# Kernel optimization log

Hardware: AMD Instinct MI355X
Metric: run time of the kernel (lower is better)

Reference implementation:

```python
import jax, jax.numpy as jnp
import numpy as np

RADIUS = 0.8
NSAMPLE = 32
EPS = 1e-5  # BatchNorm eps


def _bn(x, gamma, beta, axes):
    # BatchNorm (training-mode batch statistics), channel dim kept via broadcasting
    m = jnp.mean(x, axis=axes, keepdims=True)
    v = jnp.var(x, axis=axes, keepdims=True)
    return (x - m) * jax.lax.rsqrt(v + EPS) * gamma + beta


def setup_inputs() -> dict:
    key = jax.random.key(0)
    ks = jax.random.split(key, 6)
    B, N, P, C, COUT = 4, 8192, 2048, 128, 256
    ffps_xyz = jax.random.uniform(ks[0], (B, P, 3), dtype=jnp.float32) * 2.0 - 1.0
    backbone_xyz = jax.random.uniform(ks[1], (B, N, 3), dtype=jnp.float32) * 2.0 - 1.0
    backbone_features = jax.random.normal(ks[2], (B, C, N), dtype=jnp.float32)
    w_shift = jax.random.normal(ks[3], (3, 3), dtype=jnp.float32) * 0.1
    gamma_shift = jnp.ones((3,), jnp.float32)
    beta_shift = jnp.zeros((3,), jnp.float32)
    w_mlp = jax.random.normal(ks[4], (COUT, 3 + C), dtype=jnp.float32) * 0.05
    gamma_mlp = jnp.ones((COUT,), jnp.float32)
    beta_mlp = jnp.zeros((COUT,), jnp.float32)
    return {
        "ffps_xyz": ffps_xyz,
        "backbone_xyz": backbone_xyz,
        "backbone_features": backbone_features,
        "w_shift": w_shift,
        "gamma_shift": gamma_shift,
        "beta_shift": beta_shift,
        "w_mlp": w_mlp,
        "gamma_mlp": gamma_mlp,
        "beta_mlp": beta_mlp,
    }


def reference(ffps_xyz, backbone_xyz, backbone_features,
              w_shift, gamma_shift, beta_shift,
              w_mlp, gamma_mlp, beta_mlp):
    B, P, _ = ffps_xyz.shape
    N = backbone_xyz.shape[1]

    # ---- shift_layer: Conv1d(3->3, k=1, no bias) + BN1d + ReLU on (B,3,P) ----
    x = jnp.einsum('oc,bpc->bop', w_shift, ffps_xyz)                  # (B,3,P)
    x = _bn(x, gamma_shift[None, :, None], beta_shift[None, :, None], (0, 2))
    new_xyz = jax.nn.relu(x).transpose(0, 2, 1)                       # (B,P,3) query centers

    # ---- QueryAndGroup: ball query (radius, nsample), use_xyz=True ----
    d2 = jnp.sum((new_xyz[:, :, None, :] - backbone_xyz[:, None, :, :]) ** 2, -1)  # (B,P,N)
    within = d2 < (RADIUS * RADIUS)
    # pick the first NSAMPLE in-radius indices (CUDA ball_query semantics)
    keyv = jnp.where(within, jnp.arange(N, dtype=jnp.int32), jnp.int32(N))
    negk, idx = jax.lax.top_k(-keyv, NSAMPLE)                          # smallest keys first
    valid = (-negk) < N
    idx = jnp.where(valid, idx, idx[..., :1])                          # pad with first found idx

    g_xyz = jnp.take_along_axis(backbone_xyz[:, None, :, :], idx[..., None], axis=2)
    g_xyz = g_xyz - new_xyz[:, :, None, :]                             # (B,P,S,3) recentered
    feats = backbone_features.transpose(0, 2, 1)                       # (B,N,C)
    g_f = jnp.take_along_axis(feats[:, None, :, :], idx[..., None], axis=2)  # (B,P,S,C)
    g = jnp.concatenate([g_xyz, g_f], axis=-1)                         # (B,P,S,3+C)

    # ---- mlp: 1x1 conv (3+C -> COUT, no bias) + BN + ReLU ----
    y = jnp.einsum('oc,bpsc->bops', w_mlp, g)                          # (B,COUT,P,S)
    y = _bn(y, gamma_mlp[None, :, None, None], beta_mlp[None, :, None, None], (0, 2, 3))
    y = jax.nn.relu(y)

    # ---- max-pool over neighbor axis, squeeze, transpose ----
    y = jnp.max(y, axis=3)                                             # (B,COUT,P)
    return y.transpose(0, 2, 1)                                        # (B,P,COUT)
```

## Files before the change

kernel.cpp:

```cpp
#include <hip/hip_runtime.h>
#include <math.h>

namespace {
constexpr int B    = 4;
constexpr int N    = 8192;
constexpr int P    = 2048;
constexpr int C    = 128;
constexpr int COUT = 256;
constexpr int NS   = 32;
constexpr int BP   = B * P;
constexpr int BPB  = 2;
constexpr int GRP  = 8;
constexpr int NBLK = (BP / (BPB * GRP)) * 2;

constexpr size_t OFF_FEATT = 0;
constexpr size_t OFF_WSWZ  = 8388608;
constexpr size_t OFF_SSLOT = 8470528;
constexpr size_t OFF_SUMS  = 8471040;
constexpr size_t OFF_IDX   = 8475136;
constexpr size_t OFF_GX    = 9523712;
constexpr size_t OFF_YMAX  = 11620864;
constexpr size_t WS_NEED   = 20009472;
}

typedef short bf16x8 __attribute__((ext_vector_type(8)));
typedef float f32x4  __attribute__((ext_vector_type(4)));

typedef const __attribute__((address_space(1))) void gas_void;
typedef __attribute__((address_space(3))) void las_void;
#define GLOBAL_LOAD_LDS16(gp, lp) \
    __builtin_amdgcn_global_load_lds((gas_void*)(gp), (las_void*)(lp), 16, 0, 0)

__device__ inline unsigned short f2bf(float f) {
    unsigned u = __float_as_uint(f);
    unsigned r = u + 0x7fffu + ((u >> 16) & 1u);
    return (unsigned short)(r >> 16);
}

__global__ __launch_bounds__(256) void k_prep(const float* __restrict__ ffps,
                                              const float* __restrict__ wsh,
                                              double* __restrict__ sslot,
                                              float* __restrict__ sums) {
#pragma clang fp contract(off)
    int blk = blockIdx.x, t = threadIdx.x;
    if (blk == 8) {
        ((f32x4*)sums)[t & 127] = (f32x4){0.f, 0.f, 0.f, 0.f};
        return;
    }
    __shared__ double red[6][256];
    double w[9];
#pragma unroll
    for (int i = 0; i < 9; i++) w[i] = (double)wsh[i];
    double s[3] = {0, 0, 0}, sq[3] = {0, 0, 0};
#pragma unroll
    for (int i = 0; i < 4; i++) {
        int p = blk * 1024 + t + 256 * i;
        double f0 = (double)ffps[p * 3 + 0];
        double f1 = (double)ffps[p * 3 + 1];
        double f2 = (double)ffps[p * 3 + 2];
#pragma unroll
        for (int o = 0; o < 3; o++) {
            double xo = (w[o * 3 + 0] * f0 + w[o * 3 + 1] * f1) + w[o * 3 + 2] * f2;
            s[o] += xo;
            sq[o] += xo * xo;
        }
    }
#pragma unroll
    for (int o = 0; o < 3; o++) { red[o][t] = s[o]; red[3 + o][t] = sq[o]; }
    for (int off = 128; off > 0; off >>= 1) {
        __syncthreads();
        if (t < off) {
#pragma unroll
            for (int j = 0; j < 6; j++) red[j][t] += red[j][t + off];
        }
    }
    __syncthreads();
    if (t < 6) sslot[blk * 6 + t] = red[t][0];
}

__global__ __launch_bounds__(256) void k_front(const float* __restrict__ ffps,
                                               const float* __restrict__ bbxyz,
                                               const float* __restrict__ feat,
                                               const float* __restrict__ wsh,
                                               const float* __restrict__ gsh,
                                               const float* __restrict__ bsh,
                                               const float* __restrict__ wml,
                                               const double* __restrict__ sslot,
                                               unsigned short* __restrict__ featT,
                                               unsigned short* __restrict__ wswz,
                                               int* __restrict__ idxo,
                                               uint2* __restrict__ gxo) {
#pragma clang fp contract(off)
    int blk = blockIdx.x, t = threadIdx.x;
    if (blk >= 2048) {
        int rb = blk - 2048;
        if (rb < 2048) {
            __shared__ float tile[64][33];
            int tx = t & 31, ty = t >> 5;
            int n0 = (rb & 255) * 32, c0 = ((rb >> 8) & 1) * 64, b = rb >> 9;
            const float* src = feat + ((size_t)b * C + c0) * N + n0;
#pragma unroll
            for (int j = 0; j < 8; j++) tile[ty + 8 * j][tx] = src[(size_t)(ty + 8 * j) * N + tx];
            __syncthreads();
            int n = t >> 3;
            int k8 = (t & 7) * 8;
            unsigned vv[4];
#pragma unroll
            for (int i = 0; i < 4; i++) {
                unsigned lo = f2bf(tile[k8 + 2 * i][n]);
                unsigned hi = f2bf(tile[k8 + 2 * i + 1][n]);
                vv[i] = lo | (hi << 16);
            }
            *(int4*)&featT[((size_t)b * N + n0 + n) * C + c0 + k8] =
                make_int4((int)vv[0], (int)vv[1], (int)vv[2], (int)vv[3]);
        } else {
            int i = (rb - 2048) * 256 + t;
            int j = i & 7;
            int lane = (i >> 3) & 63;
            int rest = i >> 9;
            int ks = rest % 5, rt = rest / 5;
            int cout = rt * 16 + (lane & 15);
            int k = ks * 32 + (lane >> 4) * 8 + j;
            float v = 0.f;
            if (k < 128) v = wml[cout * 131 + 3 + k];
            else if (k < 131) v = wml[cout * 131 + (k - 128)];
            wswz[i] = f2bf(v);
        }
        return;
    }

    __shared__ double spar[6];
    if (t < 6) {
        double a = 0.0;
        for (int r = 0; r < 8; r++) a += sslot[r * 6 + t];
        spar[t] = a;
    }
    __syncthreads();
    int wv = t >> 6, lane = t & 63;
    int q = blk * 4 + wv;
    int b = q >> 11;
    double f0 = (double)ffps[q * 3 + 0];
    double f1 = (double)ffps[q * 3 + 1];
    double f2 = (double)ffps[q * 3 + 2];
    double qd[3];
#pragma unroll
    for (int o = 0; o < 3; o++) {
        double m  = spar[o] * (1.0 / 8192.0);
        double v  = spar[3 + o] * (1.0 / 8192.0) - m * m;
        double is = 1.0 / sqrt(v + 1e-5);
        double x  = ((double)wsh[o * 3 + 0] * f0 + (double)wsh[o * 3 + 1] * f1) +
                    (double)wsh[o * 3 + 2] * f2;
        double y  = ((x - m) * is) * (double)gsh[o] + (double)bsh[o];
        qd[o] = (y > 0.0) ? y : 0.0;
    }
    double qx = qd[0], qy = qd[1], qz = qd[2];
    float cfx = (float)qx, cfy = (float)qy, cfz = (float)qz;
    const float* base = bbxyz + (size_t)b * N * 3;
    const double R2 = 0.8 * 0.8;
    const float R2F = 0.64f;
    {
        double ex = fmax(fmax(qx - 1.0, -1.0 - qx), 0.0);
        double ey = fmax(fmax(qy - 1.0, -1.0 - qy), 0.0);
        double ez = fmax(fmax(qz - 1.0, -1.0 - qz), 0.0);
        if (ex * ex + ey * ey + ez * ez >= R2) {
            if (lane < NS) {
                idxo[q * NS + lane] = 0;
                float rx = base[0] - cfx, ry = base[1] - cfy, rz = base[2] - cfz;
                unsigned u01 = (unsigned)f2bf(rx) | ((unsigned)f2bf(ry) << 16);
                gxo[q * NS + lane] = make_uint2(u01, (unsigned)f2bf(rz));
            }
            return;
        }
    }
    int found = 0, firstn = -1;

    float X0[8], Y0[8], Z0[8], X1[8], Y1[8], Z1[8], X2[8], Y2[8], Z2[8];

    auto loadb = [&](float (&XX)[8], float (&YY)[8], float (&ZZ)[8], int it) {
#pragma unroll
        for (int j = 0; j < 8; j++) {
            int n = it * 512 + j * 64 + lane;
            XX[j] = base[n * 3 + 0];
            YY[j] = base[n * 3 + 1];
            ZZ[j] = base[n * 3 + 2];
        }
    };
    auto proc = [&](float (&XX)[8], float (&YY)[8], float (&ZZ)[8], int it) {
#pragma clang fp contract(off)
#pragma unroll
        for (int j = 0; j < 8; j++) {
            int n = it * 512 + j * 64 + lane;
            float dxf = cfx - XX[j];
            float dyf = cfy - YY[j];
            float dzf = cfz - ZZ[j];
            float d2f = (dxf * dxf + dyf * dyf) + dzf * dzf;
            bool within;
            if (__builtin_expect(fabsf(d2f - R2F) < 1e-4f, 0)) {
                double dx = qx - (double)XX[j];
                double dy = qy - (double)YY[j];
                double dz = qz - (double)ZZ[j];
                within = ((dx * dx + dy * dy) + dz * dz) < R2;
            } else {
                within = d2f < R2F;
            }
            unsigned long long mask = __ballot(within);
            if (firstn < 0 && mask != 0ull) firstn = (n - lane) + (__ffsll(mask) - 1);
            if (within) {
                int rank = found + __popcll(mask & ((1ull << lane) - 1ull));
                if (rank < NS) {
                    idxo[q * NS + rank] = n;
                    float rx = XX[j] - cfx, ry = YY[j] - cfy, rz = ZZ[j] - cfz;
                    unsigned u01 = (unsigned)f2bf(rx) | ((unsigned)f2bf(ry) << 16);
                    gxo[q * NS + rank] = make_uint2(u01, (unsigned)f2bf(rz));
                }
            }
            found += __popcll(mask);
        }
    };

    loadb(X0, Y0, Z0, 0);
    loadb(X1, Y1, Z1, 1);
    loadb(X2, Y2, Z2, 2);

    for (int itb = 0; itb < 16; itb += 3) {
        proc(X0, Y0, Z0, itb);
        if (found >= NS) break;
        loadb(X0, Y0, Z0, (itb + 3 < 16) ? itb + 3 : 0);
        if (itb + 1 >= 16) break;
        proc(X1, Y1, Z1, itb + 1);
        if (found >= NS) break;
        loadb(X1, Y1, Z1, (itb + 4 < 16) ? itb + 4 : 0);
        if (itb + 2 >= 16) break;
        proc(X2, Y2, Z2, itb + 2);
        if (found >= NS) break;
        loadb(X2, Y2, Z2, (itb + 5 < 16) ? itb + 5 : 0);
    }
    if (found < NS) {
        int padv = (found == 0) ? 0 : firstn;
        if (lane >= found && lane < NS) {
            idxo[q * NS + lane] = padv;
            float rx = base[padv * 3 + 0] - cfx;
            float ry = base[padv * 3 + 1] - cfy;
            float rz = base[padv * 3 + 2] - cfz;
            unsigned u01 = (unsigned)f2bf(rx) | ((unsigned)f2bf(ry) << 16);
            gxo[q * NS + lane] = make_uint2(u01, (unsigned)f2bf(rz));
        }
    }
}

__global__ __launch_bounds__(256, 4) void k_mlp_mfma(
        const unsigned short* __restrict__ featT,
        const unsigned short* __restrict__ wswz,
        const int* __restrict__ idx,
        const uint2* __restrict__ gxyz,
        float* __restrict__ ymax,
        float* __restrict__ sums) {
    __shared__ alignas(16) unsigned short G[2][4 * 4 * 64 * 8];
    int t = threadIdx.x, lane = t & 63, w = t >> 6;
    int q = lane >> 4, c16 = lane & 15;
    int blk = blockIdx.x;
    int nh = blk & 1;
    int bpbase = (blk >> 1) * (BPB * GRP);
    const bf16x8* wp = (const bf16x8*)wswz;

    bf16x8 wreg[5][2];
#pragma unroll
    for (int ks = 0; ks < 5; ks++)
#pragma unroll
        for (int nt = 0; nt < 2; nt++)
            wreg[ks][nt] = wp[((nh * 8 + w * 2 + nt) * 5 + ks) * 64 + lane];

    int sOff = (w >> 1) * NS + (w & 1) * 16 + c16;
    size_t fb = (size_t)(bpbase >> 11) * N * C;

    int nS0 = idx[bpbase * NS + sOff] & (N - 1);
    int nS1 = idx[(bpbase + BPB) * NS + sOff] & (N - 1);
    uint2 gx_c[4] = {}, gx_n[4] = {};
    if (q == 0)
#pragma unroll
        for (int mt = 0; mt < 4; mt++)
            gx_c[mt] = gxyz[(bpbase + (mt >> 1)) * NS + (mt & 1) * 16 + c16];
    {
        const unsigned short* row = featT + fb + (size_t)nS0 * C + q * 8;
#pragma unroll
        for (int ks = 0; ks < 4; ks++)
            GLOBAL_LOAD_LDS16(row + ks * 32, &G[0][(w * 4 + ks) * 512]);
    }

    float smA[2] = {0.f, 0.f}, sqA[2] = {0.f, 0.f};

    for (int g = 0; g < GRP; g++) {
        int buf = g & 1;
        int bp0 = bpbase + g * BPB;
        __syncthreads();
        if (g + 1 < GRP) {
            const unsigned short* row = featT + fb + (size_t)nS1 * C + q * 8;
#pragma unroll
            for (int ks = 0; ks < 4; ks++)
                GLOBAL_LOAD_LDS16(row + ks * 32, &G[buf ^ 1][(w * 4 + ks) * 512]);
            if (q == 0)
#pragma unroll
                for (int mt = 0; mt < 4; mt++)
                    gx_n[mt] = gxyz[(bp0 + BPB + (mt >> 1)) * NS + (mt & 1) * 16 + c16];
        }
        if (g + 2 < GRP) nS0 = idx[(bp0 + 2 * BPB) * NS + sOff] & (N - 1);

        f32x4 acc[4][2];
#pragma unroll
        for (int mt = 0; mt < 4; mt++)
#pragma unroll
            for (int nt = 0; nt < 2; nt++) acc[mt][nt] = (f32x4){0.f, 0.f, 0.f, 0.f};

#pragma unroll
        for (int ks = 0; ks < 4; ks++) {
            bf16x8 ag[4];
#pragma unroll
            for (int mt = 0; mt < 4; mt++)
                ag[mt] = *(const bf16x8*)&G[buf][((mt * 4 + ks) * 64 + lane) * 8];
#pragma unroll
            for (int nt = 0; nt < 2; nt++)
#pragma unroll
                for (int mt = 0; mt < 4; mt++)
                    acc[mt][nt] = __builtin_amdgcn_mfma_f32_16x16x32_bf16(ag[mt], wreg[ks][nt], acc[mt][nt], 0, 0, 0);
        }
        {
            bf16x8 agx[4];
#pragma unroll
            for (int mt = 0; mt < 4; mt++) {
                union { int4 i; bf16x8 h; } u;
                u.i = make_int4(q == 0 ? (int)gx_c[mt].x : 0,
                                q == 0 ? (int)gx_c[mt].y : 0, 0, 0);
                agx[mt] = u.h;
            }
#pragma unroll
            for (int nt = 0; nt < 2; nt++)
#pragma unroll
                for (int mt = 0; mt < 4; mt++)
                    acc[mt][nt] = __builtin_amdgcn_mfma_f32_16x16x32_bf16(agx[mt], wreg[4][nt], acc[mt][nt], 0, 0, 0);
        }

#pragma unroll
        for (int pm = 0; pm < BPB; pm++) {
            int bp = bp0 + pm;
#pragma unroll
            for (int nt = 0; nt < 2; nt++) {
                f32x4 a = acc[2 * pm][nt], c = acc[2 * pm + 1][nt];
                float mx = fmaxf(fmaxf(fmaxf(a[0], a[1]), fmaxf(a[2], a[3])),
                                 fmaxf(fmaxf(c[0], c[1]), fmaxf(c[2], c[3])));
                smA[nt] += ((a[0] + a[1]) + (a[2] + a[3])) + ((c[0] + c[1]) + (c[2] + c[3]));
                sqA[nt] += ((a[0] * a[0] + a[1] * a[1]) + (a[2] * a[2] + a[3] * a[3])) +
                           ((c[0] * c[0] + c[1] * c[1]) + (c[2] * c[2] + c[3] * c[3]));
                mx = fmaxf(mx, __shfl_xor(mx, 16, 64));
                mx = fmaxf(mx, __shfl_xor(mx, 32, 64));
                if (q == 0)
                    ymax[(size_t)bp * COUT + nh * 128 + w * 32 + nt * 16 + c16] = mx;
            }
        }
        nS1 = nS0;
#pragma unroll
        for (int mt = 0; mt < 4; mt++) gx_c[mt] = gx_n[mt];
    }

#pragma unroll
    for (int nt = 0; nt < 2; nt++) {
        float sm = smA[nt], sq = sqA[nt];
        sm += __shfl_xor(sm, 16, 64);
        sm += __shfl_xor(sm, 32, 64);
        sq += __shfl_xor(sq, 16, 64);
        sq += __shfl_xor(sq, 32, 64);
        if (q == 0) {
            int cout = nh * 128 + w * 32 + nt * 16 + c16;
            atomicAdd(&sums[cout], sm);
            atomicAdd(&sums[256 + cout], sq);
        }
    }
}

__global__ __launch_bounds__(256) void k_final(const float* __restrict__ ymax,
                                               const float* __restrict__ sums,
                                               const float* __restrict__ gam,
                                               const float* __restrict__ bet,
                                               float* __restrict__ out) {
    __shared__ float sa[256], sb[256];
    int t = threadIdx.x;
    {
        double sm = (double)sums[t], sq = (double)sums[256 + t];
        double mean = sm * (1.0 / 262144.0);
        double var = sq * (1.0 / 262144.0) - mean * mean;
        double a = (double)gam[t] / sqrt(var + 1e-5);
        sa[t] = (float)a;
        sb[t] = (float)((double)bet[t] - mean * a);
    }
    __syncthreads();
    int i = blockIdx.x * 256 + t;
    int c0 = (t & 63) * 4;
    f32x4 y = *(const f32x4*)&ymax[(size_t)i * 4];
    f32x4 r;
#pragma unroll
    for (int j = 0; j < 4; j++) r[j] = fmaxf(sa[c0 + j] * y[j] + sb[c0 + j], 0.f);
    *(f32x4*)&out[(size_t)i * 4] = r;
}

extern "C" void kernel_launch(void* const* d_in, const int* in_sizes, int n_in,
                              void* d_out, int out_size, void* d_ws, size_t ws_size,
                              hipStream_t stream) {
    const float* ffps  = (const float*)d_in[0];
    const float* bbxyz = (const float*)d_in[1];
    const float* feat  = (const float*)d_in[2];
    const float* wsh   = (const float*)d_in[3];
    const float* gsh   = (const float*)d_in[4];
    const float* bsh   = (const float*)d_in[5];
    const float* wml   = (const float*)d_in[6];
    const float* gml   = (const float*)d_in[7];
    const float* bml   = (const float*)d_in[8];
    float* out = (float*)d_out;
    char* ws = (char*)d_ws;
    if (ws_size < WS_NEED) return;

    unsigned short* featT = (unsigned short*)(ws + OFF_FEATT);
    unsigned short* wswz  = (unsigned short*)(ws + OFF_WSWZ);
    double*         sslot = (double*)(ws + OFF_SSLOT);
    float*          sums  = (float*)(ws + OFF_SUMS);
    int*            idx   = (int*)(ws + OFF_IDX);
    uint2*          gx    = (uint2*)(ws + OFF_GX);
    float*          ymax  = (float*)(ws + OFF_YMAX);

    k_prep<<<dim3(9), dim3(256), 0, stream>>>(ffps, wsh, sslot, sums);
    k_front<<<dim3(2048 + 2048 + 160), dim3(256), 0, stream>>>(
        ffps, bbxyz, feat, wsh, gsh, bsh, wml, sslot, featT, wswz, idx, gx);
    k_mlp_mfma<<<dim3(NBLK), dim3(256), 0, stream>>>(featT, wswz, idx, gx, ymax, sums);
    k_final<<<dim3(BP * COUT / 1024), dim3(256), 0, stream>>>(ymax, sums, gml, bml, out);
}
```

Measured before the change: 155.5 us.

## Fuse all stages into one cooperative kernel with grid syncs

Replaces the four separate launches (prep, front, mlp, final) with a single cooperative mega-kernel that runs each stage in turn, separated by grid-wide barriers. Shared memory is reused across stages through a union. The goal is to remove inter-kernel launch gaps and tail effects. In exchange, every block waits at each grid sync, and the work is redistributed with some imbalance, since a few blocks carry leftover transpose units. It falls back to the old launches if the cooperative launch fails.

Result: slower. 569.7 us (+266.4%).

```diff
diff --git a/kernel.cpp b/kernel.cpp
--- a/kernel.cpp
+++ b/kernel.cpp
@@ -1,5 +1,8 @@
 #include <hip/hip_runtime.h>
+#include <hip/hip_cooperative_groups.h>
 #include <math.h>
+
+namespace cg = cooperative_groups;
 
 namespace {
 constexpr int B    = 4;
@@ -35,6 +38,370 @@
     unsigned u = __float_as_uint(f);
     unsigned r = u + 0x7fffu + ((u >> 16) & 1u);
     return (unsigned short)(r >> 16);
+}
+
+
+union MegaSh {
+    float tile[64][33];
+    double red[6][256];
+    unsigned short G[2][8192];
+};
+
+__global__ __launch_bounds__(256, 4) void k_mega(
+        const float* __restrict__ ffps,
+        const float* __restrict__ bbxyz,
+        const float* __restrict__ feat,
+        const float* __restrict__ wsh,
+        const float* __restrict__ gsh,
+        const float* __restrict__ bsh,
+        const float* __restrict__ wml,
+        const float* __restrict__ gam,
+        const float* __restrict__ bet,
+        float* __restrict__ out,
+        unsigned short* __restrict__ featT,
+        unsigned short* __restrict__ wswz,
+        double* __restrict__ sslot,
+        float* __restrict__ sums,
+        int* __restrict__ idxo,
+        uint2* __restrict__ gxo,
+        float* __restrict__ ymax) {
+#pragma clang fp contract(off)
+    cg::grid_group grid = cg::this_grid();
+    __shared__ alignas(16) MegaSh sh;
+    __shared__ double spar[6];
+    __shared__ float sa[256], sb[256];
+    int blk = blockIdx.x, t = threadIdx.x;
+
+    auto transpose_unit = [&](int rb) {
+        int tx = t & 31, ty = t >> 5;
+        int n0 = (rb & 255) * 32, c0 = ((rb >> 8) & 1) * 64, b = rb >> 9;
+        const float* src = feat + ((size_t)b * C + c0) * N + n0;
+        __syncthreads();
+#pragma unroll
+        for (int j = 0; j < 8; j++) sh.tile[ty + 8 * j][tx] = src[(size_t)(ty + 8 * j) * N + tx];
+        __syncthreads();
+        int n = t >> 3;
+        int k8 = (t & 7) * 8;
+        unsigned vv[4];
+#pragma unroll
+        for (int i = 0; i < 4; i++) {
+            unsigned lo = f2bf(sh.tile[k8 + 2 * i][n]);
+            unsigned hi = f2bf(sh.tile[k8 + 2 * i + 1][n]);
+            vv[i] = lo | (hi << 16);
+        }
+        *(int4*)&featT[((size_t)b * N + n0 + n) * C + c0 + k8] =
+            make_int4((int)vv[0], (int)vv[1], (int)vv[2], (int)vv[3]);
+    };
+
+    if (blk < 8) {
+        double w[9];
+#pragma unroll
+        for (int i = 0; i < 9; i++) w[i] = (double)wsh[i];
+        double s[3] = {0, 0, 0}, sq[3] = {0, 0, 0};
+#pragma unroll
+        for (int i = 0; i < 4; i++) {
+            int p = blk * 1024 + t + 256 * i;
+            double f0 = (double)ffps[p * 3 + 0];
+            double f1 = (double)ffps[p * 3 + 1];
+            double f2 = (double)ffps[p * 3 + 2];
+#pragma unroll
+            for (int o = 0; o < 3; o++) {
+                double xo = (w[o * 3 + 0] * f0 + w[o * 3 + 1] * f1) + w[o * 3 + 2] * f2;
+                s[o] += xo;
+                sq[o] += xo * xo;
+            }
+        }
+#pragma unroll
+        for (int o = 0; o < 3; o++) { sh.red[o][t] = s[o]; sh.red[3 + o][t] = sq[o]; }
+        for (int off = 128; off > 0; off >>= 1) {
+            __syncthreads();
+            if (t < off) {
+#pragma unroll
+                for (int j = 0; j < 6; j++) sh.red[j][t] += sh.red[j][t + off];
+            }
+        }
+        __syncthreads();
+        if (t < 6) sslot[blk * 6 + t] = sh.red[t][0];
+    } else if (blk == 8) {
+        if (t < 128) ((f32x4*)sums)[t] = (f32x4){0.f, 0.f, 0.f, 0.f};
+    } else {
+        transpose_unit((blk - 9) * 2);
+        transpose_unit((blk - 9) * 2 + 1);
+    }
+    if (blk < 160) {
+        int i = blk * 256 + t;
+        int j = i & 7;
+        int lane = (i >> 3) & 63;
+        int rest = i >> 9;
+        int ks = rest % 5, rt = rest / 5;
+        int cout = rt * 16 + (lane & 15);
+        int k = ks * 32 + (lane >> 4) * 8 + j;
+        float v = 0.f;
+        if (k < 128) v = wml[cout * 131 + 3 + k];
+        else if (k < 131) v = wml[cout * 131 + (k - 128)];
+        wswz[i] = f2bf(v);
+    }
+    grid.sync();
+
+    if (blk < 9) {
+        transpose_unit(2030 + blk * 2);
+        transpose_unit(2030 + blk * 2 + 1);
+    }
+    if (t < 6) {
+        double a = 0.0;
+        for (int r = 0; r < 8; r++) a += sslot[r * 6 + t];
+        spar[t] = a;
+    }
+    __syncthreads();
+    {
+        int wv = t >> 6, lane = t & 63;
+        int qbase = (blk >> 1) * 16 + (blk & 1) * 8;
+        for (int qi = 0; qi < 2; qi++) {
+            int q = qbase + wv * 2 + qi;
+            double f0 = (double)ffps[q * 3 + 0];
+            double f1 = (double)ffps[q * 3 + 1];
+            double f2 = (double)ffps[q * 3 + 2];
+            double qd[3];
+#pragma unroll
+            for (int o = 0; o < 3; o++) {
+                double m  = spar[o] * (1.0 / 8192.0);
+                double v  = spar[3 + o] * (1.0 / 8192.0) - m * m;
+                double is = 1.0 / sqrt(v + 1e-5);
+                double x  = ((double)wsh[o * 3 + 0] * f0 + (double)wsh[o * 3 + 1] * f1) +
+                            (double)wsh[o * 3 + 2] * f2;
+                double y  = ((x - m) * is) * (double)gsh[o] + (double)bsh[o];
+                qd[o] = (y > 0.0) ? y : 0.0;
+            }
+            double qx = qd[0], qy = qd[1], qz = qd[2];
+            float cfx = (float)qx, cfy = (float)qy, cfz = (float)qz;
+            const float* base = bbxyz + (size_t)(q >> 11) * N * 3;
+            const double R2 = 0.8 * 0.8;
+            const float R2F = 0.64f;
+            double ex = fmax(fmax(qx - 1.0, -1.0 - qx), 0.0);
+            double ey = fmax(fmax(qy - 1.0, -1.0 - qy), 0.0);
+            double ez = fmax(fmax(qz - 1.0, -1.0 - qz), 0.0);
+            if (ex * ex + ey * ey + ez * ez >= R2) {
+                if (lane < NS) {
+                    idxo[q * NS + lane] = 0;
+                    float rx = base[0] - cfx, ry = base[1] - cfy, rz = base[2] - cfz;
+                    unsigned u01 = (unsigned)f2bf(rx) | ((unsigned)f2bf(ry) << 16);
+                    gxo[q * NS + lane] = make_uint2(u01, (unsigned)f2bf(rz));
+                }
+                continue;
+            }
+            int found = 0, firstn = -1;
+            float X0[8], Y0[8], Z0[8], X1[8], Y1[8], Z1[8], X2[8], Y2[8], Z2[8];
+            auto loadb = [&](float (&XX)[8], float (&YY)[8], float (&ZZ)[8], int it) {
+#pragma unroll
+                for (int j = 0; j < 8; j++) {
+                    int n = it * 512 + j * 64 + lane;
+                    XX[j] = base[n * 3 + 0];
+                    YY[j] = base[n * 3 + 1];
+                    ZZ[j] = base[n * 3 + 2];
+                }
+            };
+            auto proc = [&](float (&XX)[8], float (&YY)[8], float (&ZZ)[8], int it) {
+#pragma clang fp contract(off)
+#pragma unroll
+                for (int j = 0; j < 8; j++) {
+                    int n = it * 512 + j * 64 + lane;
+                    float dxf = cfx - XX[j];
+                    float dyf = cfy - YY[j];
+                    float dzf = cfz - ZZ[j];
+                    float d2f = (dxf * dxf + dyf * dyf) + dzf * dzf;
+                    bool within;
+                    if (__builtin_expect(fabsf(d2f - R2F) < 1e-4f, 0)) {
+                        double dx = qx - (double)XX[j];
+                        double dy = qy - (double)YY[j];
+                        double dz = qz - (double)ZZ[j];
+                        within = ((dx * dx + dy * dy) + dz * dz) < R2;
+                    } else {
+                        within = d2f < R2F;
+                    }
+                    unsigned long long mask = __ballot(within);
+                    if (firstn < 0 && mask != 0ull) firstn = (n - lane) + (__ffsll(mask) - 1);
+                    if (within) {
+                        int rank = found + __popcll(mask & ((1ull << lane) - 1ull));
+                        if (rank < NS) {
+                            idxo[q * NS + rank] = n;
+                            float rx = XX[j] - cfx, ry = YY[j] - cfy, rz = ZZ[j] - cfz;
+                            unsigned u01 = (unsigned)f2bf(rx) | ((unsigned)f2bf(ry) << 16);
+                            gxo[q * NS + rank] = make_uint2(u01, (unsigned)f2bf(rz));
+                        }
+                    }
+                    found += __popcll(mask);
+                }
+            };
+            loadb(X0, Y0, Z0, 0);
+            loadb(X1, Y1, Z1, 1);
+            loadb(X2, Y2, Z2, 2);
+            for (int itb = 0; itb < 16; itb += 3) {
+                proc(X0, Y0, Z0, itb);
+                if (found >= NS) break;
+                loadb(X0, Y0, Z0, (itb + 3 < 16) ? itb + 3 : 0);
+                if (itb + 1 >= 16) break;
+                proc(X1, Y1, Z1, itb + 1);
+                if (found >= NS) break;
+                loadb(X1, Y1, Z1, (itb + 4 < 16) ? itb + 4 : 0);
+                if (itb + 2 >= 16) break;
+                proc(X2, Y2, Z2, itb + 2);
+                if (found >= NS) break;
+                loadb(X2, Y2, Z2, (itb + 5 < 16) ? itb + 5 : 0);
+            }
+            if (found < NS) {
+                int padv = (found == 0) ? 0 : firstn;
+                if (lane >= found && lane < NS) {
+                    idxo[q * NS + lane] = padv;
+                    float rx = base[padv * 3 + 0] - cfx;
+                    float ry = base[padv * 3 + 1] - cfy;
+                    float rz = base[padv * 3 + 2] - cfz;
+                    unsigned u01 = (unsigned)f2bf(rx) | ((unsigned)f2bf(ry) << 16);
+                    gxo[q * NS + lane] = make_uint2(u01, (unsigned)f2bf(rz));
+                }
+            }
+        }
+    }
+    grid.sync();
+
+    {
+        int lane = t & 63, w = t >> 6;
+        int q = lane >> 4, c16 = lane & 15;
+        int nh = blk & 1;
+        int bpbase = (blk >> 1) * (BPB * GRP);
+        const bf16x8* wp = (const bf16x8*)wswz;
+        bf16x8 wreg[5][2];
+#pragma unroll
+        for (int ks = 0; ks < 5; ks++)
+#pragma unroll
+            for (int nt = 0; nt < 2; nt++)
+                wreg[ks][nt] = wp[((nh * 8 + w * 2 + nt) * 5 + ks) * 64 + lane];
+
+        int sOff = (w >> 1) * NS + (w & 1) * 16 + c16;
+        size_t fb = (size_t)(bpbase >> 11) * N * C;
+
+        int nS0 = idxo[bpbase * NS + sOff] & (N - 1);
+        int nS1 = idxo[(bpbase + BPB) * NS + sOff] & (N - 1);
+        uint2 gx_c[4] = {}, gx_n[4] = {};
+        if (q == 0)
+#pragma unroll
+            for (int mt = 0; mt < 4; mt++)
+                gx_c[mt] = gxo[(bpbase + (mt >> 1)) * NS + (mt & 1) * 16 + c16];
+        {
+            const unsigned short* row = featT + fb + (size_t)nS0 * C + q * 8;
+#pragma unroll
+            for (int ks = 0; ks < 4; ks++)
+                GLOBAL_LOAD_LDS16(row + ks * 32, &sh.G[0][(w * 4 + ks) * 512]);
+        }
+
+        float smA[2] = {0.f, 0.f}, sqA[2] = {0.f, 0.f};
+
+        for (int g = 0; g < GRP; g++) {
+            int buf = g & 1;
+            int bp0 = bpbase + g * BPB;
+            __syncthreads();
+            if (g + 1 < GRP) {
+                const unsigned short* row = featT + fb + (size_t)nS1 * C + q * 8;
+#pragma unroll
+                for (int ks = 0; ks < 4; ks++)
+                    GLOBAL_LOAD_LDS16(row + ks * 32, &sh.G[buf ^ 1][(w * 4 + ks) * 512]);
+                if (q == 0)
+#pragma unroll
+                    for (int mt = 0; mt < 4; mt++)
+                        gx_n[mt] = gxo[(bp0 + BPB + (mt >> 1)) * NS + (mt & 1) * 16 + c16];
+            }
+            if (g + 2 < GRP) nS0 = idxo[(bp0 + 2 * BPB) * NS + sOff] & (N - 1);
+
+            f32x4 acc[4][2];
+#pragma unroll
+            for (int mt = 0; mt < 4; mt++)
+#pragma unroll
+                for (int nt = 0; nt < 2; nt++) acc[mt][nt] = (f32x4){0.f, 0.f, 0.f, 0.f};
+
+#pragma unroll
+            for (int ks = 0; ks < 4; ks++) {
+                bf16x8 ag[4];
+#pragma unroll
+                for (int mt = 0; mt < 4; mt++)
+                    ag[mt] = *(const bf16x8*)&sh.G[buf][((mt * 4 + ks) * 64 + lane) * 8];
+#pragma unroll
+                for (int nt = 0; nt < 2; nt++)
+#pragma unroll
+                    for (int mt = 0; mt < 4; mt++)
+                        acc[mt][nt] = __builtin_amdgcn_mfma_f32_16x16x32_bf16(ag[mt], wreg[ks][nt], acc[mt][nt], 0, 0, 0);
+            }
+            {
+                bf16x8 agx[4];
+#pragma unroll
+                for (int mt = 0; mt < 4; mt++) {
+                    union { int4 i; bf16x8 h; } u;
+                    u.i = make_int4(q == 0 ? (int)gx_c[mt].x : 0,
+                                    q == 0 ? (int)gx_c[mt].y : 0, 0, 0);
+                    agx[mt] = u.h;
+                }
+#pragma unroll
+                for (int nt = 0; nt < 2; nt++)
+#pragma unroll
+                    for (int mt = 0; mt < 4; mt++)
+                        acc[mt][nt] = __builtin_amdgcn_mfma_f32_16x16x32_bf16(agx[mt], wreg[4][nt], acc[mt][nt], 0, 0, 0);
+            }
+
+#pragma unroll
+            for (int pm = 0; pm < BPB; pm++) {
+                int bp = bp0 + pm;
+#pragma unroll
+                for (int nt = 0; nt < 2; nt++) {
+                    f32x4 a = acc[2 * pm][nt], c = acc[2 * pm + 1][nt];
+                    float mx = fmaxf(fmaxf(fmaxf(a[0], a[1]), fmaxf(a[2], a[3])),
+                                     fmaxf(fmaxf(c[0], c[1]), fmaxf(c[2], c[3])));
+                    smA[nt] += ((a[0] + a[1]) + (a[2] + a[3])) + ((c[0] + c[1]) + (c[2] + c[3]));
+                    sqA[nt] += ((a[0] * a[0] + a[1] * a[1]) + (a[2] * a[2] + a[3] * a[3])) +
+                               ((c[0] * c[0] + c[1] * c[1]) + (c[2] * c[2] + c[3] * c[3]));
+                    mx = fmaxf(mx, __shfl_xor(mx, 16, 64));
+                    mx = fmaxf(mx, __shfl_xor(mx, 32, 64));
+                    if (q == 0)
+                        ymax[(size_t)bp * COUT + nh * 128 + w * 32 + nt * 16 + c16] = mx;
+                }
+            }
+            nS1 = nS0;
+#pragma unroll
+            for (int mt = 0; mt < 4; mt++) gx_c[mt] = gx_n[mt];
+        }
+
+#pragma unroll
+        for (int nt = 0; nt < 2; nt++) {
+            float sm = smA[nt], sq = sqA[nt];
+            sm += __shfl_xor(sm, 16, 64);
+            sm += __shfl_xor(sm, 32, 64);
+            sq += __shfl_xor(sq, 16, 64);
+            sq += __shfl_xor(sq, 32, 64);
+            if (q == 0) {
+                int cout = nh * 128 + w * 32 + nt * 16 + c16;
+                atomicAdd(&sums[cout], sm);
+                atomicAdd(&sums[256 + cout], sq);
+            }
+        }
+    }
+    grid.sync();
+
+    {
+        double sm = (double)sums[t], sq = (double)sums[256 + t];
+        double mean = sm * (1.0 / 262144.0);
+        double var = sq * (1.0 / 262144.0) - mean * mean;
+        double a = (double)gam[t] / sqrt(var + 1e-5);
+        sa[t] = (float)a;
+        sb[t] = (float)((double)bet[t] - mean * a);
+    }
+    __syncthreads();
+#pragma unroll
+    for (int u = 0; u < 2; u++) {
+        int i = blk * 512 + u * 256 + t;
+        int c0 = (t & 63) * 4;
+        f32x4 y = *(const f32x4*)&ymax[(size_t)i * 4];
+        f32x4 r;
+#pragma unroll
+        for (int j = 0; j < 4; j++) r[j] = fmaxf(sa[c0 + j] * y[j] + sb[c0 + j], 0.f);
+        *(f32x4*)&out[(size_t)i * 4] = r;
+    }
 }
 
 __global__ __launch_bounds__(256) void k_prep(const float* __restrict__ ffps,
@@ -128,7 +495,6 @@
         }
         return;
     }
-
     __shared__ double spar[6];
     if (t < 6) {
         double a = 0.0;
@@ -173,9 +539,7 @@
         }
     }
     int found = 0, firstn = -1;
-
     float X0[8], Y0[8], Z0[8], X1[8], Y1[8], Z1[8], X2[8], Y2[8], Z2[8];
-
     auto loadb = [&](float (&XX)[8], float (&YY)[8], float (&ZZ)[8], int it) {
 #pragma unroll
         for (int j = 0; j < 8; j++) {
@@ -217,11 +581,9 @@
             found += __popcll(mask);
         }
     };
-
     loadb(X0, Y0, Z0, 0);
     loadb(X1, Y1, Z1, 1);
     loadb(X2, Y2, Z2, 2);
-
     for (int itb = 0; itb < 16; itb += 3) {
         proc(X0, Y0, Z0, itb);
         if (found >= NS) break;
@@ -262,17 +624,14 @@
     int nh = blk & 1;
     int bpbase = (blk >> 1) * (BPB * GRP);
     const bf16x8* wp = (const bf16x8*)wswz;
-
     bf16x8 wreg[5][2];
 #pragma unroll
     for (int ks = 0; ks < 5; ks++)
 #pragma unroll
         for (int nt = 0; nt < 2; nt++)
             wreg[ks][nt] = wp[((nh * 8 + w * 2 + nt) * 5 + ks) * 64 + lane];
-
     int sOff = (w >> 1) * NS + (w & 1) * 16 + c16;
     size_t fb = (size_t)(bpbase >> 11) * N * C;
-
     int nS0 = idx[bpbase * NS + sOff] & (N - 1);
     int nS1 = idx[(bpbase + BPB) * NS + sOff] & (N - 1);
     uint2 gx_c[4] = {}, gx_n[4] = {};
@@ -286,9 +645,7 @@
         for (int ks = 0; ks < 4; ks++)
             GLOBAL_LOAD_LDS16(row + ks * 32, &G[0][(w * 4 + ks) * 512]);
     }
-
     float smA[2] = {0.f, 0.f}, sqA[2] = {0.f, 0.f};
-
     for (int g = 0; g < GRP; g++) {
         int buf = g & 1;
         int bp0 = bpbase + g * BPB;
@@ -304,13 +661,11 @@
                     gx_n[mt] = gxyz[(bp0 + BPB + (mt >> 1)) * NS + (mt & 1) * 16 + c16];
         }
         if (g + 2 < GRP) nS0 = idx[(bp0 + 2 * BPB) * NS + sOff] & (N - 1);
-
         f32x4 acc[4][2];
 #pragma unroll
         for (int mt = 0; mt < 4; mt++)
 #pragma unroll
             for (int nt = 0; nt < 2; nt++) acc[mt][nt] = (f32x4){0.f, 0.f, 0.f, 0.f};
-
 #pragma unroll
         for (int ks = 0; ks < 4; ks++) {
             bf16x8 ag[4];
@@ -338,7 +693,6 @@
                 for (int mt = 0; mt < 4; mt++)
                     acc[mt][nt] = __builtin_amdgcn_mfma_f32_16x16x32_bf16(agx[mt], wreg[4][nt], acc[mt][nt], 0, 0, 0);
         }
-
 #pragma unroll
         for (int pm = 0; pm < BPB; pm++) {
             int bp = bp0 + pm;
@@ -360,7 +714,6 @@
 #pragma unroll
         for (int mt = 0; mt < 4; mt++) gx_c[mt] = gx_n[mt];
     }
-
 #pragma unroll
     for (int nt = 0; nt < 2; nt++) {
         float sm = smA[nt], sq = sqA[nt];
@@ -425,9 +778,18 @@
     uint2*          gx    = (uint2*)(ws + OFF_GX);
     float*          ymax  = (float*)(ws + OFF_YMAX);
 
-    k_prep<<<dim3(9), dim3(256), 0, stream>>>(ffps, wsh, sslot, sums);
-    k_front<<<dim3(2048 + 2048 + 160), dim3(256), 0, stream>>>(
-        ffps, bbxyz, feat, wsh, gsh, bsh, wml, sslot, featT, wswz, idx, gx);
-    k_mlp_mfma<<<dim3(NBLK), dim3(256), 0, stream>>>(featT, wswz, idx, gx, ymax, sums);
-    k_final<<<dim3(BP * COUT / 1024), dim3(256), 0, stream>>>(ymax, sums, gml, bml, out);
+    void* kargs[] = {(void*)&ffps, (void*)&bbxyz, (void*)&feat, (void*)&wsh,
+                     (void*)&gsh,  (void*)&bsh,   (void*)&wml,  (void*)&gml,
+                     (void*)&bml,  (void*)&out,   (void*)&featT, (void*)&wswz,
+                     (void*)&sslot, (void*)&sums, (void*)&idx,  (void*)&gx,
+                     (void*)&ymax};
+    hipError_t err = hipLaunchCooperativeKernel((const void*)k_mega, dim3(1024),
+                                                dim3(256), kargs, 0, stream);
+    if (err != hipSuccess) {
+        k_prep<<<dim3(9), dim3(256), 0, stream>>>(ffps, wsh, sslot, sums);
+        k_front<<<dim3(2048 + 2048 + 160), dim3(256), 0, stream>>>(
+            ffps, bbxyz, feat, wsh, gsh, bsh, wml, sslot, featT, wswz, idx, gx);
+        k_mlp_mfma<<<dim3(NBLK), dim3(256), 0, stream>>>(featT, wswz, idx, gx, ymax, sums);
+        k_final<<<dim3(BP * COUT / 1024), dim3(256), 0, stream>>>(ymax, sums, gml, bml, out);
+    }
 }
```
